# Kernel optimization log

Measured on AMD Instinct MI355X. Metric: run time of the kernel, lower is better.

Reference implementation:

```python
import jax, jax.numpy as jnp
import numpy as np

N = 16384
C_IN = 128
C_OUT = 128
S_DIM = 4
P_DIM = 32
K = 16


def setup_inputs() -> dict:
    key = jax.random.key(0)
    ks = jax.random.split(key, 8)
    lim = lambda fan_in: 1.0 / np.sqrt(fan_in)
    u = lambda k_, shape, b: jax.random.uniform(k_, shape, jnp.float32, -b, b)
    return {
        "x": jax.random.normal(ks[0], (N, C_IN), jnp.float32),
        "Ws": u(ks[1], (S_DIM, C_IN), lim(C_IN)),
        "bs": u(ks[2], (S_DIM,), lim(C_IN)),
        "Wh": u(ks[3], (P_DIM, C_IN), lim(C_IN)),
        "bh": u(ks[4], (P_DIM,), lim(C_IN)),
        "W1": u(ks[5], (C_OUT, C_IN), lim(C_IN)),
        "W2": u(ks[6], (C_OUT, 2 * P_DIM), lim(2 * P_DIM)),
        "b2": u(ks[7], (C_OUT,), lim(2 * P_DIM)),
        "k": K,
    }


def reference(x, Ws, bs, Wh, bh, W1, W2, b2, k):
    # latent space positions and message vectors
    s = x @ Ws.T + bs            # [N, S]
    h = x @ Wh.T + bh            # [N, P]
    # squared-distance matrix via Gram trick (monotone in true distance,
    # so k-NN indices match torch.cdist + topk(largest=False))
    sq = jnp.sum(s * s, axis=-1)                         # [N]
    d2 = sq[:, None] + sq[None, :] - 2.0 * (s @ s.T)     # [N, N]
    _, idx = jax.lax.top_k(-d2, k)                       # [N, k] neighbour ids (incl. self)
    # exact squared latent distance to selected neighbours (as in torch code)
    s_j = s[idx]                                          # [N, k, S]
    w = jnp.exp(-10.0 * jnp.sum((s[:, None, :] - s_j) ** 2, axis=-1))  # [N, k]
    msg = h[idx] * w[..., None]                           # [N, k, P]
    agg = jnp.concatenate([msg.mean(axis=1), msg.max(axis=1)], axis=-1)  # [N, 2P]
    return x @ W1.T + agg @ W2.T + b2                     # [N, C_OUT]
```

## Files before the change

kernel.cpp:

```cpp
#include <hip/hip_runtime.h>
#include <hip/hip_bf16.h>


#define NPTS 16384
#define CIN  128
#define SD   4
#define PD   32
#define KNN  16
#define COUT 128
#define FLTMAX 3.4028234663852886e+38f
#define NBIN 33
#define QPB  8
#define QCAP 512
#define MCAP 128

typedef float v2f __attribute__((ext_vector_type(2)));
typedef unsigned int uint;
typedef unsigned long long u64;

#define WS_S4     0
#define WS_H      0x40000
#define WS_AGG_M  0x280000
#define WS_WT_M   0x680000
#define WS_T2     0x6A0000
#define WS_MASK   0x700000
#define WS_NEED_M 0x2700000
#define WS_CJ_F   0x400000
#define WS_AGG_F  0xC00000
#define WS_WT_F   0x1000000
#define JS   16
#define TJF  (NPTS/JS)

__device__ __forceinline__ float d2f(const float4 a, const float4 b) {
  v2f d0 = {a.x - b.x, a.y - b.y};
  v2f d1 = {a.z - b.z, a.w - b.w};
  v2f pr = d0*d0 + d1*d1;
  return pr.x + pr.y;
}

__global__ __launch_bounds__(256) void k1_proj(
    const float* __restrict__ x, const float* __restrict__ Ws, const float* __restrict__ bs,
    const float* __restrict__ Wh, const float* __restrict__ bh,
    float4* __restrict__ s4, float* __restrict__ h) {
  __shared__ float  lw[36*128];
  __shared__ float  lx[64*132];
  __shared__ double rs[3*64*5];
  __shared__ float  rh[3*64*33];
  const int t = threadIdx.x;
  const int row0 = blockIdx.x * 64;
  for (int i2 = t; i2 < 36*128; i2 += 256)
    lw[i2] = (i2 < 512) ? Ws[i2] : Wh[i2 - 512];
#pragma unroll
  for (int g = 0; g < 8; ++g) {
    int fi = g*256 + t;
    int r = fi >> 5, c4 = fi & 31;
    *(float4*)&lx[r*132 + c4*4] = *(const float4*)&x[(size_t)(row0 + r)*CIN + c4*4];
  }
  __syncthreads();
  const int kq = t >> 6;
  const int r  = t & 63;
  const int kb = kq * 32;
  double sacc[4] = {0.0, 0.0, 0.0, 0.0};
  float  hacc[32];
#pragma unroll
  for (int p = 0; p < 32; ++p) hacc[p] = 0.f;
#pragma unroll
  for (int k4 = 0; k4 < 8; ++k4) {
    float4 xv = *(const float4*)&lx[r*132 + kb + k4*4];
    int kg = kb + k4*4;
#pragma unroll
    for (int p = 0; p < 4; ++p) {
      float4 wv = *(const float4*)&lw[p*128 + kg];
      sacc[p] = fma((double)xv.x, (double)wv.x, sacc[p]);
      sacc[p] = fma((double)xv.y, (double)wv.y, sacc[p]);
      sacc[p] = fma((double)xv.z, (double)wv.z, sacc[p]);
      sacc[p] = fma((double)xv.w, (double)wv.w, sacc[p]);
    }
#pragma unroll
    for (int p = 0; p < 32; ++p) {
      float4 wv = *(const float4*)&lw[(4+p)*128 + kg];
      hacc[p] = fmaf(xv.x, wv.x, fmaf(xv.y, wv.y, fmaf(xv.z, wv.z, fmaf(xv.w, wv.w, hacc[p]))));
    }
  }
  if (kq > 0) {
    const int bq = kq - 1;
#pragma unroll
    for (int d = 0; d < 4; ++d) rs[(bq*64 + r)*5 + d] = sacc[d];
#pragma unroll
    for (int p = 0; p < 32; ++p) rh[(bq*64 + r)*33 + p] = hacc[p];
  }
  __syncthreads();
  if (kq == 0) {
    const int row = row0 + r;
    float so[4];
#pragma unroll
    for (int d = 0; d < 4; ++d) {
      double sd = sacc[d] + rs[(0*64 + r)*5 + d] + rs[(1*64 + r)*5 + d]
                + rs[(2*64 + r)*5 + d] + (double)bs[d];
      so[d] = (float)sd;
    }
    s4[row] = make_float4(so[0], so[1], so[2], so[3]);
#pragma unroll
    for (int p4 = 0; p4 < 8; ++p4) {
      float o[4];
#pragma unroll
      for (int c = 0; c < 4; ++c) {
        int p = p4*4 + c;
        o[c] = hacc[p] + rh[(0*64 + r)*33 + p] + rh[(1*64 + r)*33 + p]
             + rh[(2*64 + r)*33 + p] + bh[p];
      }
      *(float4*)&h[(size_t)row*PD + p4*4] = make_float4(o[0], o[1], o[2], o[3]);
    }
  }
}

__global__ __launch_bounds__(256) void k2t_thresh(
    const float4* __restrict__ s4, float* __restrict__ t2) {
  __shared__ float4 tile[2064];
  __shared__ uint   lhist[256*NBIN];
  const int t = threadIdx.x;
#pragma unroll
  for (int g = 0; g < 8; ++g) {
    int j = g*256 + t;
    tile[j + (j >> 7)] = s4[j];
  }
#pragma unroll
  for (int b = 0; b < NBIN; ++b) lhist[t*NBIN + b] = 0u;
  const int ql = t >> 4, tq = t & 15;
  const int q  = blockIdx.x*16 + ql;
  const float4 sq = s4[q];
  __syncthreads();
  float tau = d2f(sq, tile[tq*129]);
#pragma unroll
  for (int m = 1; m < 16; m <<= 1) tau = fmaxf(tau, __shfl_xor(tau, m, 16));
  const int ktop = (int)(__float_as_uint(tau) >> 21);
  const int hb = t*NBIN;
#pragma unroll 4
  for (int u = 0; u < 128; ++u) {
    float4 p = tile[tq*129 + u];
    float e = d2f(sq, p);
    int key = (int)(__float_as_uint(e) >> 21);
    int rel = ktop - key;
    rel = rel < 0 ? 0 : (rel > 32 ? 32 : rel);
    atomicAdd(&lhist[hb + rel], 1u);
  }
  __syncthreads();
  uint c0 = 0, c1 = 0;
  const int qb = ql*16;
  for (int u = 0; u < 16; ++u) {
    c0 += lhist[(qb + u)*NBIN + tq*2];
    c1 += (tq*2 + 1 < NBIN) ? lhist[(qb + u)*NBIN + tq*2 + 1] : 0u;
  }
  int S = (int)(c0 + c1);
#pragma unroll
  for (int d = 1; d < 16; d <<= 1) {
    int v = __shfl_down(S, d, 16);
    S += (tq + d < 16) ? v : 0;
  }
  int g = -1;
  if (S >= KNN) g = 2*tq;
  if (S - (int)c0 >= KNN) g = 2*tq + 1;
#pragma unroll
  for (int m = 1; m < 16; m <<= 1) g = max(g, __shfl_xor(g, m, 16));
  if (tq == 0) {
    uint K = (uint)(ktop - g);
    t2[q] = __uint_as_float((K << 21) | 0x1FFFFFu);
  }
}

__global__ __launch_bounds__(256) void k2b_mask(
    const float4* __restrict__ s4, const float* __restrict__ t2, uint* __restrict__ maskw) {
  __shared__ float4 tile4[128];
  __shared__ float  tileb[128];
  const int t  = threadIdx.x;
  const int c  = blockIdx.x >> 4;
  const int ig = blockIdx.x & 15;
  if (t < 128) {
    float4 p = s4[c*128 + t];
    tile4[t] = p;
    tileb[t] = 0.5f*(p.x*p.x + p.y*p.y + p.z*p.z + p.w*p.w);
  }
  const int q0 = ig*1024 + t;
  v2f sxy[4], szw[4]; float ui[4];
#pragma unroll
  for (int m = 0; m < 4; ++m) {
    int q = q0 + m*256;
    float4 s = s4[q];
    sxy[m] = (v2f){s.x, s.y};
    szw[m] = (v2f){s.z, s.w};
    float n2 = s.x*s.x + s.y*s.y + s.z*s.z + s.w*s.w;
    ui[m] = 0.5f*(n2 - t2[q]) - 4e-6f;
  }
  __syncthreads();
#pragma unroll 1
  for (int w = 0; w < 4; ++w) {
    uint msk[4] = {0u, 0u, 0u, 0u};
#pragma unroll
    for (int bit = 31; bit >= 0; --bit) {
      float4 p = tile4[w*32 + bit];
      float nb = tileb[w*32 + bit];
      v2f pxy = (v2f){p.x, p.y};
      v2f pzw = (v2f){p.z, p.w};
      v2f nb2 = (v2f){-nb, 0.f};
#pragma unroll
      for (int m = 0; m < 4; ++m) {
        v2f a = szw[m]*pzw + nb2;
        v2f b = sxy[m]*pxy + a;
        float val = b.x + b.y;
        msk[m] = msk[m] + msk[m] + (val >= ui[m] ? 1u : 0u);
      }
    }
#pragma unroll
    for (int m = 0; m < 4; ++m) {
      int q = q0 + m*256;
      maskw[((size_t)c*NPTS + q)*4 + w] = msk[m];
    }
  }
}

__global__ __launch_bounds__(256) void k3_sel2(
    const float4* __restrict__ s4, const float* __restrict__ h,
    const uint4* __restrict__ maskw, float* __restrict__ agg) {
  __shared__ u64  qbuf[QPB*MCAP];
  __shared__ u64  keys[QPB*QCAP];
  __shared__ u64  win[QPB*KNN];
  __shared__ uint hist[QPB*32];
  __shared__ uint cnts[QPB];
  __shared__ uint mc[QPB];
  unsigned short* jl = (unsigned short*)qbuf;
  const int t  = threadIdx.x;
  const int ql = t >> 5, ln = t & 31;
  const int q  = blockIdx.x*QPB + ql;
  if (ln == 0) { cnts[ql] = 0u; mc[ql] = 0u; }
  hist[ql*32 + ln] = 0u;
  if (ln < KNN) win[ql*KNN + ln] = 0ull;
  const float4 sq = s4[q];
  __syncthreads();
  uint wv[16]; int pc = 0;
#pragma unroll
  for (int u = 0; u < 4; ++u) {
    const int c = ln*4 + u;
    uint4 m4 = maskw[(size_t)c*NPTS + q];
    wv[u*4+0] = m4.x; wv[u*4+1] = m4.y; wv[u*4+2] = m4.z; wv[u*4+3] = m4.w;
    pc += __popc(m4.x) + __popc(m4.y) + __popc(m4.z) + __popc(m4.w);
  }
  int base = (int)atomicAdd(&cnts[ql], (uint)pc);
#pragma unroll
  for (int w = 0; w < 16; ++w) {
    uint bits = wv[w];
    const int jb = (ln*4 + (w >> 2))*128 + (w & 3)*32;
    while (bits) {
      int b = __builtin_ctz(bits); bits &= bits - 1;
      if (base < QCAP) jl[ql*QCAP + base] = (unsigned short)(jb + b);
      ++base;
    }
  }
  __syncthreads();
  const int cnt = min((int)cnts[ql], QCAP);
  uint kmax = 0u;
  for (int u = ln; u < cnt; u += 32) {
    int j = jl[ql*QCAP + u];
    float e = d2f(sq, s4[j]);
    uint db = __float_as_uint(e);
    keys[ql*QCAP + u] = ((u64)db << 14) | (uint)j;
    kmax = max(kmax, db >> 21);
  }
#pragma unroll
  for (int m = 1; m < 32; m <<= 1) kmax = max(kmax, (uint)__shfl_xor((int)kmax, m, 32));
  for (int u = ln; u < cnt; u += 32) {
    uint cls = (uint)(keys[ql*QCAP + u] >> 35);
    uint rel = min(kmax - cls, 31u);
    atomicAdd(&hist[ql*32 + rel], 1u);
  }
  __syncthreads();
  uint cum = hist[ql*32 + ln];
#pragma unroll
  for (int d = 1; d < 32; d <<= 1) {
    uint v = (uint)__shfl_down((int)cum, d, 32);
    if (ln + d < 32) cum += v;
  }
  const uint need = (uint)(cnt < KNN ? cnt : KNN);
  u64 bal = __ballot(cum >= need);
  uint half = (uint)(bal >> (((t >> 5) & 1) * 32));
  const uint rstar = 31u - (uint)__builtin_clz(half);
  const uint bcls = kmax - rstar;
  __syncthreads();
  for (int u = ln; u < cnt; u += 32) {
    u64 key = keys[ql*QCAP + u];
    if ((uint)(key >> 35) <= bcls) {
      uint pos = atomicAdd(&mc[ql], 1u);
      if (pos < MCAP) qbuf[ql*MCAP + pos] = key;
    }
  }
  __syncthreads();
  const int mcnt = (int)mc[ql];
  if (mcnt <= MCAP) {
    for (int w = ln; w < mcnt; w += 32) {
      u64 key = qbuf[ql*MCAP + w];
      int rank = 0;
      for (int v = 0; v < mcnt; ++v) rank += (qbuf[ql*MCAP + v] < key) ? 1 : 0;
      if (rank < KNN) win[ql*KNN + rank] = key;
    }
  } else {
    for (int u = ln; u < cnt; u += 32) {
      u64 key = keys[ql*QCAP + u];
      if ((uint)(key >> 35) <= bcls) {
        int rank = 0;
        for (int v = 0; v < cnt; ++v) rank += (keys[ql*QCAP + v] < key) ? 1 : 0;
        if (rank < KNN) win[ql*KNN + rank] = key;
      }
    }
  }
  __syncthreads();
  float sum = 0.f, mx = -FLTMAX;
#pragma unroll 1
  for (int r = 0; r < KNN; ++r) {
    u64 key = win[ql*KNN + r];
    float d2 = __uint_as_float((uint)(key >> 14));
    int j = (int)(key & 16383u);
    float w = __expf(-10.f * d2);
    float m = w * h[(size_t)j*PD + ln];
    sum += m; mx = fmaxf(mx, m);
  }
  agg[(size_t)q*64 + ln]      = sum * 0.0625f;
  agg[(size_t)q*64 + 32 + ln] = mx;
}

__global__ __launch_bounds__(256) void k2_knn_fb(
    const float4* __restrict__ s4, unsigned short* __restrict__ cand_j) {
  __shared__ float4 tile[TJF];
  __shared__ int    lbuf[256*33];
  const int t  = threadIdx.x;
  const int ib = blockIdx.x & 31;
  const int jc = blockIdx.x >> 5;
  const int jbase = jc * TJF;
#pragma unroll
  for (int g = 0; g < 4; ++g) tile[g*256 + t] = s4[jbase + g*256 + t];
  const int ia = ib*256 + t;
  const int ic = ia + 8192;
  const float4 sa = s4[ia];
  const float4 sc = s4[ic];
  __syncthreads();
  float va[KNN], vb[KNN]; int ja[KNN], jb[KNN];
#pragma unroll
  for (int q = 0; q < KNN; ++q) { va[q] = FLTMAX; ja[q] = 0; vb[q] = FLTMAX; jb[q] = 0; }
  float cma = FLTMAX, cmb = FLTMAX;
  int cpa = 0, cpb = 0, ca = 0, cb = 0;
  auto insertA = [&](float e, int jj) {
#pragma unroll
    for (int q = 0; q < KNN; ++q) if (q == cpa) { va[q] = e; ja[q] = jj; }
    cma = va[0]; cpa = 0;
#pragma unroll
    for (int q = 1; q < KNN; ++q) { if (va[q] > cma) { cma = va[q]; cpa = q; } }
  };
  auto insertB = [&](float e, int jj) {
#pragma unroll
    for (int q = 0; q < KNN; ++q) if (q == cpb) { vb[q] = e; jb[q] = jj; }
    cmb = vb[0]; cpb = 0;
#pragma unroll
    for (int q = 1; q < KNN; ++q) { if (vb[q] > cmb) { cmb = vb[q]; cpb = q; } }
  };
  auto compactA = [&]() {
    for (int u = 0; u < ca; ++u) {
      int jj = lbuf[t*33 + u];
      float e = d2f(sa, tile[jj]);
      if (e < cma) insertA(e, jj);
    }
    ca = 0;
  };
  auto compactB = [&]() {
    for (int u = 0; u < cb; ++u) {
      int jj = lbuf[t*33 + 16 + u];
      float e = d2f(sc, tile[jj]);
      if (e < cmb) insertB(e, jj);
    }
    cb = 0;
  };
  for (int ob = 0; ob < TJF/8; ++ob) {
#pragma unroll
    for (int u = 0; u < 8; ++u) {
      int jj = ob*8 + u;
      float4 p = tile[jj];
      float ea = d2f(sa, p);
      float eb = d2f(sc, p);
      if (ea < cma) { lbuf[t*33 + ca] = jj; ++ca; }
      if (eb < cmb) { lbuf[t*33 + 16 + cb] = jj; ++cb; }
    }
    if (__any(ca > 8)) compactA();
    if (__any(cb > 8)) compactB();
  }
  compactA(); compactB();
#pragma unroll
  for (int q = 0; q < KNN; ++q) {
    int c = jc*KNN + q;
    cand_j[(size_t)c*NPTS + ia] = (unsigned short)(ja[q] + jbase);
    cand_j[(size_t)c*NPTS + ic] = (unsigned short)(jb[q] + jbase);
  }
}

__global__ __launch_bounds__(256) void k3_merge_fb(
    const float4* __restrict__ s4, const float4* __restrict__ h4,
    const unsigned short* __restrict__ cand_j, float* __restrict__ agg) {
  __shared__ float le[64*67];
  __shared__ int   lj[64*67];
  const int t  = threadIdx.x;
  const int il = t & 63, tq = t >> 6;
  const int i  = blockIdx.x*64 + il;
  const float4 si = s4[i];
  float val[KNN]; int vid[KNN];
#pragma unroll
  for (int q = 0; q < KNN; ++q) { val[q] = FLTMAX; vid[q] = 0; }
  float cmax = FLTMAX; int cpos = 0;
  for (int u = 0; u < 64; ++u) {
    int c = tq*64 + u;
    int j = cand_j[(size_t)c*NPTS + i];
    float e = d2f(si, s4[j]);
    if (e < cmax) {
#pragma unroll
      for (int q = 0; q < KNN; ++q) if (q == cpos) { val[q] = e; vid[q] = j; }
      cmax = val[0]; cpos = 0;
#pragma unroll
      for (int q = 1; q < KNN; ++q) { if (val[q] > cmax) { cmax = val[q]; cpos = q; } }
    }
  }
#pragma unroll
  for (int q = 0; q < KNN; ++q) {
    le[il*67 + tq*16 + q] = val[q];
    lj[il*67 + tq*16 + q] = vid[q];
  }
  __syncthreads();
  if (t < 64) {
    float mv[KNN]; int mj[KNN];
#pragma unroll
    for (int q = 0; q < KNN; ++q) { mv[q] = FLTMAX; mj[q] = 0; }
    float cm2 = FLTMAX; int cp2 = 0;
    for (int u = 0; u < 64; ++u) {
      float e = le[t*67 + u];
      int   j = lj[t*67 + u];
      if (e < cm2) {
#pragma unroll
        for (int q = 0; q < KNN; ++q) if (q == cp2) { mv[q] = e; mj[q] = j; }
        cm2 = mv[0]; cp2 = 0;
#pragma unroll
        for (int q = 1; q < KNN; ++q) { if (mv[q] > cm2) { cm2 = mv[q]; cp2 = q; } }
      }
    }
#pragma unroll
    for (int q = 0; q < KNN; ++q) {
      le[t*67 + q] = __expf(-10.f * mv[q]);
      lj[t*67 + q] = mj[q];
    }
  }
  __syncthreads();
  float ms[8], mm[8];
#pragma unroll
  for (int p = 0; p < 8; ++p) { ms[p] = 0.f; mm[p] = -FLTMAX; }
#pragma unroll 1
  for (int q = 0; q < KNN; ++q) {
    float w = le[il*67 + q];
    int   j = lj[il*67 + q];
    float4 a = h4[(size_t)j*8 + tq*2];
    float4 b = h4[(size_t)j*8 + tq*2 + 1];
    float m0 = a.x*w, m1 = a.y*w, m2 = a.z*w, m3 = a.w*w;
    float m4 = b.x*w, m5 = b.y*w, m6 = b.z*w, m7 = b.w*w;
    ms[0] += m0; mm[0] = fmaxf(mm[0], m0);
    ms[1] += m1; mm[1] = fmaxf(mm[1], m1);
    ms[2] += m2; mm[2] = fmaxf(mm[2], m2);
    ms[3] += m3; mm[3] = fmaxf(mm[3], m3);
    ms[4] += m4; mm[4] = fmaxf(mm[4], m4);
    ms[5] += m5; mm[5] = fmaxf(mm[5], m5);
    ms[6] += m6; mm[6] = fmaxf(mm[6], m6);
    ms[7] += m7; mm[7] = fmaxf(mm[7], m7);
  }
  float4 o0 = make_float4(ms[0]*0.0625f, ms[1]*0.0625f, ms[2]*0.0625f, ms[3]*0.0625f);
  float4 o1 = make_float4(ms[4]*0.0625f, ms[5]*0.0625f, ms[6]*0.0625f, ms[7]*0.0625f);
  *(float4*)&agg[(size_t)i*64 + tq*8]      = o0;
  *(float4*)&agg[(size_t)i*64 + tq*8 + 4]  = o1;
  *(float4*)&agg[(size_t)i*64 + 32 + tq*8]     = make_float4(mm[0], mm[1], mm[2], mm[3]);
  *(float4*)&agg[(size_t)i*64 + 32 + tq*8 + 4] = make_float4(mm[4], mm[5], mm[6], mm[7]);
}

__global__ __launch_bounds__(256) void k4a_wt(
    const float* __restrict__ W1, const float* __restrict__ W2, float* __restrict__ wT) {
  int idx = blockIdx.x*256 + threadIdx.x;
  if (idx >= 192*COUT) return;
  int k = idx >> 7, c = idx & 127;
  float v = (k < 128) ? W1[(size_t)c*128 + k] : W2[(size_t)c*64 + (k - 128)];
  wT[(size_t)k*COUT + c] = v;
}

__global__ __launch_bounds__(256) void k4_out2(
    const float* __restrict__ x, const float* __restrict__ agg,
    const float* __restrict__ wT, const float* __restrict__ b2,
    float* __restrict__ out) {
  __shared__ float xa[32*192];
  const int t = threadIdx.x;
  const int row0 = blockIdx.x * 32;
#pragma unroll
  for (int g = 0; g < 4; ++g) {
    int fi = g*256 + t;
    int r = fi >> 5, c4 = fi & 31;
    *(float4*)&xa[r*192 + c4*4] = *(const float4*)&x[(size_t)(row0+r)*CIN + c4*4];
  }
#pragma unroll
  for (int g = 0; g < 2; ++g) {
    int fi = g*256 + t;
    int r = fi >> 4, c4 = fi & 15;
    *(float4*)&xa[r*192 + 128 + c4*4] = *(const float4*)&agg[(size_t)(row0+r)*64 + c4*4];
  }
  __syncthreads();
  const int c4 = t & 31;
  const int rg = t >> 5;
  float acc[4][4];
#pragma unroll
  for (int r = 0; r < 4; ++r) { acc[r][0]=0.f; acc[r][1]=0.f; acc[r][2]=0.f; acc[r][3]=0.f; }
  for (int k = 0; k < 192; k += 4) {
    float4 w0 = *(const float4*)&wT[(size_t)(k+0)*COUT + c4*4];
    float4 w1 = *(const float4*)&wT[(size_t)(k+1)*COUT + c4*4];
    float4 w2 = *(const float4*)&wT[(size_t)(k+2)*COUT + c4*4];
    float4 w3 = *(const float4*)&wT[(size_t)(k+3)*COUT + c4*4];
#pragma unroll
    for (int r = 0; r < 4; ++r) {
      float4 xv = *(const float4*)&xa[(rg*4 + r)*192 + k];
      acc[r][0] = fmaf(xv.x, w0.x, fmaf(xv.y, w1.x, fmaf(xv.z, w2.x, fmaf(xv.w, w3.x, acc[r][0]))));
      acc[r][1] = fmaf(xv.x, w0.y, fmaf(xv.y, w1.y, fmaf(xv.z, w2.y, fmaf(xv.w, w3.y, acc[r][1]))));
      acc[r][2] = fmaf(xv.x, w0.z, fmaf(xv.y, w1.z, fmaf(xv.z, w2.z, fmaf(xv.w, w3.z, acc[r][2]))));
      acc[r][3] = fmaf(xv.x, w0.w, fmaf(xv.y, w1.w, fmaf(xv.z, w2.w, fmaf(xv.w, w3.w, acc[r][3]))));
    }
  }
  float4 bias = *(const float4*)&b2[c4*4];
#pragma unroll
  for (int r = 0; r < 4; ++r) {
    float4 o = make_float4(acc[r][0]+bias.x, acc[r][1]+bias.y, acc[r][2]+bias.z, acc[r][3]+bias.w);
    *(float4*)&out[(size_t)(row0 + rg*4 + r)*COUT + c4*4] = o;
  }
}

extern "C" void kernel_launch(void* const* d_in, const int* in_sizes, int n_in,
                              void* d_out, int out_size, void* d_ws, size_t ws_size,
                              hipStream_t stream) {
  const float* x  = (const float*)d_in[0];
  const float* Ws = (const float*)d_in[1];
  const float* bs = (const float*)d_in[2];
  const float* Wh = (const float*)d_in[3];
  const float* bh = (const float*)d_in[4];
  const float* W1 = (const float*)d_in[5];
  const float* W2 = (const float*)d_in[6];
  const float* b2 = (const float*)d_in[7];
  float* out = (float*)d_out;

  char* ws = (char*)d_ws;
  float4* s4 = (float4*)(ws + WS_S4);
  float*  h  = (float*) (ws + WS_H);

  k1_proj<<<NPTS/64, 256, 0, stream>>>(x, Ws, bs, Wh, bh, s4, h);

  if (ws_size >= (size_t)WS_NEED_M) {
    float* t2  = (float*)(ws + WS_T2);
    float* agg = (float*)(ws + WS_AGG_M);
    float* wT  = (float*)(ws + WS_WT_M);
    uint*  mw  = (uint*) (ws + WS_MASK);
    k2t_thresh<<<NPTS/16, 256, 0, stream>>>(s4, t2);
    k2b_mask<<<2048, 256, 0, stream>>>(s4, t2, mw);
    k3_sel2<<<NPTS/QPB, 256, 0, stream>>>(s4, h, (const uint4*)mw, agg);
    k4a_wt<<<(192*COUT + 255)/256, 256, 0, stream>>>(W1, W2, wT);
    k4_out2<<<NPTS/32, 256, 0, stream>>>(x, agg, wT, b2, out);
  } else {
    unsigned short* cj = (unsigned short*)(ws + WS_CJ_F);
    float* agg = (float*)(ws + WS_AGG_F);
    float* wT  = (float*)(ws + WS_WT_F);
    k2_knn_fb<<<512, 256, 0, stream>>>(s4, cj);
    k3_merge_fb<<<NPTS/64, 256, 0, stream>>>(s4, (const float4*)h, cj, agg);
    k4a_wt<<<(192*COUT + 255)/256, 256, 0, stream>>>(W1, W2, wT);
    k4_out2<<<NPTS/32, 256, 0, stream>>>(x, agg, wT, b2, out);
  }
}
```

Before: 220.9 us.

## Emit candidate index lists with global atomics instead of a dense bitmask

The mask kernel now extracts set bits itself and appends candidate indices to a per-query global list through global atomic counters, replacing the 32 MB dense bitmask that the selection kernel previously read and compacted. The selection kernel reads the compact candidate list directly and drops one block barrier. The distance accumulation is rewritten as scalar fma chains in place of packed v2f math. This costs a memset and many global atomics with scattered 2-byte writes, and candidate order becomes nondeterministic.

```diff
diff --git a/kernel.cpp b/kernel.cpp
--- a/kernel.cpp
+++ b/kernel.cpp
@@ -20,11 +20,12 @@
 
 #define WS_S4     0
 #define WS_H      0x40000
-#define WS_AGG_M  0x280000
-#define WS_WT_M   0x680000
-#define WS_T2     0x6A0000
-#define WS_MASK   0x700000
-#define WS_NEED_M 0x2700000
+#define WS_T2     0x240000
+#define WS_CNT    0x250000
+#define WS_WT     0x260000
+#define WS_AGG    0x280000
+#define WS_CAND   0x680000
+#define WS_NEED   0x1680000
 #define WS_CJ_F   0x400000
 #define WS_AGG_F  0xC00000
 #define WS_WT_F   0x1000000
@@ -168,8 +169,9 @@
   }
 }
 
-__global__ __launch_bounds__(256) void k2b_mask(
-    const float4* __restrict__ s4, const float* __restrict__ t2, uint* __restrict__ maskw) {
+__global__ __launch_bounds__(256) void k2b_ext(
+    const float4* __restrict__ s4, const float* __restrict__ t2,
+    uint* __restrict__ cnt, unsigned short* __restrict__ cand) {
   __shared__ float4 tile4[128];
   __shared__ float  tileb[128];
   const int t  = threadIdx.x;
@@ -181,85 +183,71 @@
     tileb[t] = 0.5f*(p.x*p.x + p.y*p.y + p.z*p.z + p.w*p.w);
   }
   const int q0 = ig*1024 + t;
-  v2f sxy[4], szw[4]; float ui[4];
+  float4 sq[4]; float ui[4];
 #pragma unroll
   for (int m = 0; m < 4; ++m) {
     int q = q0 + m*256;
     float4 s = s4[q];
-    sxy[m] = (v2f){s.x, s.y};
-    szw[m] = (v2f){s.z, s.w};
+    sq[m] = s;
     float n2 = s.x*s.x + s.y*s.y + s.z*s.z + s.w*s.w;
     ui[m] = 0.5f*(n2 - t2[q]) - 4e-6f;
   }
   __syncthreads();
+  uint msk[4][4];
 #pragma unroll 1
   for (int w = 0; w < 4; ++w) {
-    uint msk[4] = {0u, 0u, 0u, 0u};
+    uint mk0 = 0u, mk1 = 0u, mk2 = 0u, mk3 = 0u;
 #pragma unroll
     for (int bit = 31; bit >= 0; --bit) {
       float4 p = tile4[w*32 + bit];
       float nb = tileb[w*32 + bit];
-      v2f pxy = (v2f){p.x, p.y};
-      v2f pzw = (v2f){p.z, p.w};
-      v2f nb2 = (v2f){-nb, 0.f};
-#pragma unroll
-      for (int m = 0; m < 4; ++m) {
-        v2f a = szw[m]*pzw + nb2;
-        v2f b = sxy[m]*pxy + a;
-        float val = b.x + b.y;
-        msk[m] = msk[m] + msk[m] + (val >= ui[m] ? 1u : 0u);
+      float a0 = fmaf(sq[0].x, p.x, fmaf(sq[0].y, p.y, fmaf(sq[0].z, p.z, fmaf(sq[0].w, p.w, -nb))));
+      float a1 = fmaf(sq[1].x, p.x, fmaf(sq[1].y, p.y, fmaf(sq[1].z, p.z, fmaf(sq[1].w, p.w, -nb))));
+      float a2 = fmaf(sq[2].x, p.x, fmaf(sq[2].y, p.y, fmaf(sq[2].z, p.z, fmaf(sq[2].w, p.w, -nb))));
+      float a3 = fmaf(sq[3].x, p.x, fmaf(sq[3].y, p.y, fmaf(sq[3].z, p.z, fmaf(sq[3].w, p.w, -nb))));
+      mk0 = mk0 + mk0 + (a0 >= ui[0] ? 1u : 0u);
+      mk1 = mk1 + mk1 + (a1 >= ui[1] ? 1u : 0u);
+      mk2 = mk2 + mk2 + (a2 >= ui[2] ? 1u : 0u);
+      mk3 = mk3 + mk3 + (a3 >= ui[3] ? 1u : 0u);
+    }
+    msk[0][w] = mk0; msk[1][w] = mk1; msk[2][w] = mk2; msk[3][w] = mk3;
+  }
+#pragma unroll 1
+  for (int m = 0; m < 4; ++m) {
+    const int q = q0 + m*256;
+#pragma unroll 1
+    for (int w = 0; w < 4; ++w) {
+      uint bits = msk[m][w];
+      while (bits) {
+        int b = __builtin_ctz(bits); bits &= bits - 1;
+        uint pos = atomicAdd(&cnt[q], 1u);
+        if (pos < QCAP) cand[(size_t)q*QCAP + pos] = (unsigned short)(c*128 + w*32 + b);
       }
     }
-#pragma unroll
-    for (int m = 0; m < 4; ++m) {
-      int q = q0 + m*256;
-      maskw[((size_t)c*NPTS + q)*4 + w] = msk[m];
-    }
-  }
-}
-
-__global__ __launch_bounds__(256) void k3_sel2(
+  }
+}
+
+__global__ __launch_bounds__(256) void k3_sel3(
     const float4* __restrict__ s4, const float* __restrict__ h,
-    const uint4* __restrict__ maskw, float* __restrict__ agg) {
+    const uint* __restrict__ cntg, const unsigned short* __restrict__ cand,
+    float* __restrict__ agg) {
+  __shared__ u64  keys[QPB*QCAP];
   __shared__ u64  qbuf[QPB*MCAP];
-  __shared__ u64  keys[QPB*QCAP];
   __shared__ u64  win[QPB*KNN];
   __shared__ uint hist[QPB*32];
-  __shared__ uint cnts[QPB];
   __shared__ uint mc[QPB];
-  unsigned short* jl = (unsigned short*)qbuf;
   const int t  = threadIdx.x;
   const int ql = t >> 5, ln = t & 31;
   const int q  = blockIdx.x*QPB + ql;
-  if (ln == 0) { cnts[ql] = 0u; mc[ql] = 0u; }
+  if (ln == 0) mc[ql] = 0u;
   hist[ql*32 + ln] = 0u;
   if (ln < KNN) win[ql*KNN + ln] = 0ull;
   const float4 sq = s4[q];
-  __syncthreads();
-  uint wv[16]; int pc = 0;
-#pragma unroll
-  for (int u = 0; u < 4; ++u) {
-    const int c = ln*4 + u;
-    uint4 m4 = maskw[(size_t)c*NPTS + q];
-    wv[u*4+0] = m4.x; wv[u*4+1] = m4.y; wv[u*4+2] = m4.z; wv[u*4+3] = m4.w;
-    pc += __popc(m4.x) + __popc(m4.y) + __popc(m4.z) + __popc(m4.w);
-  }
-  int base = (int)atomicAdd(&cnts[ql], (uint)pc);
-#pragma unroll
-  for (int w = 0; w < 16; ++w) {
-    uint bits = wv[w];
-    const int jb = (ln*4 + (w >> 2))*128 + (w & 3)*32;
-    while (bits) {
-      int b = __builtin_ctz(bits); bits &= bits - 1;
-      if (base < QCAP) jl[ql*QCAP + base] = (unsigned short)(jb + b);
-      ++base;
-    }
-  }
-  __syncthreads();
-  const int cnt = min((int)cnts[ql], QCAP);
+  const int cnt = min((int)cntg[q], QCAP);
+  __syncthreads();
   uint kmax = 0u;
   for (int u = ln; u < cnt; u += 32) {
-    int j = jl[ql*QCAP + u];
+    int j = cand[(size_t)q*QCAP + u];
     float e = d2f(sq, s4[j]);
     uint db = __float_as_uint(e);
     keys[ql*QCAP + u] = ((u64)db << 14) | (uint)j;
@@ -284,7 +272,6 @@
   uint half = (uint)(bal >> (((t >> 5) & 1) * 32));
   const uint rstar = 31u - (uint)__builtin_clz(half);
   const uint bcls = kmax - rstar;
-  __syncthreads();
   for (int u = ln; u < cnt; u += 32) {
     u64 key = keys[ql*QCAP + u];
     if ((uint)(key >> 35) <= bcls) {
@@ -555,14 +542,16 @@
 
   k1_proj<<<NPTS/64, 256, 0, stream>>>(x, Ws, bs, Wh, bh, s4, h);
 
-  if (ws_size >= (size_t)WS_NEED_M) {
+  if (ws_size >= (size_t)WS_NEED) {
     float* t2  = (float*)(ws + WS_T2);
-    float* agg = (float*)(ws + WS_AGG_M);
-    float* wT  = (float*)(ws + WS_WT_M);
-    uint*  mw  = (uint*) (ws + WS_MASK);
+    uint*  cnt = (uint*) (ws + WS_CNT);
+    float* agg = (float*)(ws + WS_AGG);
+    float* wT  = (float*)(ws + WS_WT);
+    unsigned short* cand = (unsigned short*)(ws + WS_CAND);
     k2t_thresh<<<NPTS/16, 256, 0, stream>>>(s4, t2);
-    k2b_mask<<<2048, 256, 0, stream>>>(s4, t2, mw);
-    k3_sel2<<<NPTS/QPB, 256, 0, stream>>>(s4, h, (const uint4*)mw, agg);
+    hipMemsetAsync(cnt, 0, NPTS*sizeof(uint), stream);
+    k2b_ext<<<2048, 256, 0, stream>>>(s4, t2, cnt, cand);
+    k3_sel3<<<NPTS/QPB, 256, 0, stream>>>(s4, h, cnt, cand, agg);
     k4a_wt<<<(192*COUT + 255)/256, 256, 0, stream>>>(W1, W2, wT);
     k4_out2<<<NPTS/32, 256, 0, stream>>>(x, agg, wT, b2, out);
   } else {
```

After: 248.4 us. 12.4% more time.
